# Performance work log

Measured on AMD Instinct MI355X. Metric: run time of the kernel, lower is better.

## Reference

```python
import jax, jax.numpy as jnp
import numpy as np

B, S, D, H = 4, 2048, 1024, 16
HD = D // H  # head_dim = 64


def setup_inputs() -> dict:
    key = jax.random.key(0)
    ks = jax.random.split(key, 9)
    sd = 1.0 / np.sqrt(D)
    x = jax.random.normal(ks[0], (B, S, D), dtype=jnp.float32)
    Wq = jax.random.normal(ks[1], (D, D), dtype=jnp.float32) * sd
    Wk = jax.random.normal(ks[2], (D, D), dtype=jnp.float32) * sd
    Wv = jax.random.normal(ks[3], (D, D), dtype=jnp.float32) * sd
    Wo = jax.random.normal(ks[4], (D, D), dtype=jnp.float32) * sd
    bq = jax.random.normal(ks[5], (D,), dtype=jnp.float32) * sd
    bk = jax.random.normal(ks[6], (D,), dtype=jnp.float32) * sd
    bv = jax.random.normal(ks[7], (D,), dtype=jnp.float32) * sd
    bo = jax.random.normal(ks[8], (D,), dtype=jnp.float32) * sd
    return {"x": x, "Wq": Wq, "bq": bq, "Wk": Wk, "bk": bk,
            "Wv": Wv, "bv": bv, "Wo": Wo, "bo": bo}


def reference(x, Wq, bq, Wk, bk, Wv, bv, Wo, bo):
    b, s, d = x.shape
    scale = jnp.float32(np.sqrt(HD))
    # projections, split into heads: (b, h, s, hd)
    def heads(y):
        return y.reshape(b, s, H, HD).transpose(0, 2, 1, 3)
    Q = heads(x @ Wq + bq)
    K = heads(x @ Wk + bk)
    V = heads(x @ Wv + bv)
    # (b, h, s, s) scores with causal mask
    scores = jnp.einsum('bhqd,bhkd->bhqk', Q, K) / scale
    causal = jnp.tril(jnp.ones((s, s), dtype=bool))
    scores = jnp.where(causal[None, None], scores, jnp.float32(-jnp.inf))
    probs = jax.nn.softmax(scores, axis=-1)
    out = jnp.einsum('bhqk,bhkd->bhqd', probs, V)
    out = out.transpose(0, 2, 1, 3).reshape(b, s, d)
    return out @ Wo + bo
```

## Files before the change

### kernel.cpp

```cpp
#include <hip/hip_runtime.h>
#include <hip/hip_bf16.h>
#include <cstdint>

typedef __bf16 bf16x8 __attribute__((ext_vector_type(8)));
typedef float f32x4 __attribute__((ext_vector_type(4)));
typedef float f32x16 __attribute__((ext_vector_type(16)));
typedef unsigned short u16t;

__device__ __forceinline__ u16t f2bf(float f) {
    uint32_t u = __builtin_bit_cast(uint32_t, f);
    u += 0x7FFF + ((u >> 16) & 1);
    return (u16t)(u >> 16);
}

constexpr int Bb = 4, Ss = 2048, Dd = 1024, Hh = 16;
constexpr int Mrows = Bb * Ss;
constexpr float NEG = -1e30f;

__global__ __launch_bounds__(256) void cvt_bf16(const float* __restrict__ in,
                                                u16t* __restrict__ out, int n) {
    int i = (blockIdx.x * 256 + threadIdx.x) * 4;
    if (i >= n) return;
    float4 v = *(const float4*)(in + i);
    u16t o[4] = {f2bf(v.x), f2bf(v.y), f2bf(v.z), f2bf(v.w)};
    *(ushort4*)(out + i) = *(ushort4*)o;
}

__global__ __launch_bounds__(256) void transpose_cvt4(const float* __restrict__ W0, u16t* __restrict__ T0,
                                                      const float* __restrict__ W1, u16t* __restrict__ T1,
                                                      const float* __restrict__ W2, u16t* __restrict__ T2,
                                                      const float* __restrict__ W3, u16t* __restrict__ T3) {
    __shared__ float tile[64][65];
    const float* W = blockIdx.z == 0 ? W0 : blockIdx.z == 1 ? W1 : blockIdx.z == 2 ? W2 : W3;
    u16t* WT       = blockIdx.z == 0 ? T0 : blockIdx.z == 1 ? T1 : blockIdx.z == 2 ? T2 : T3;
    int n0 = blockIdx.x * 64, k0 = blockIdx.y * 64;
    int c = threadIdx.x & 63, r0 = (threadIdx.x >> 6) * 16;
    for (int i = 0; i < 16; i++)
        tile[c][r0 + i] = W[(size_t)(k0 + r0 + i) * Dd + n0 + c];
    __syncthreads();
    for (int i = 0; i < 16; i++)
        WT[(size_t)(n0 + r0 + i) * Dd + k0 + c] = f2bf(tile[r0 + i][c]);
}

__global__ __launch_bounds__(256) void gemm_bt(const u16t* __restrict__ A,
                                               const u16t* __restrict__ BT,
                                               const float* __restrict__ bias,
                                               u16t* __restrict__ outBF,
                                               float* __restrict__ outF, int mode,
                                               float oscale) {
    __shared__ __align__(16) u16t Asm[128 * 32];
    __shared__ __align__(16) u16t Bsm[128 * 32];
    int tid = threadIdx.x, lane = tid & 63, w = tid >> 6;
    int wm = w >> 1, wn = w & 1;
    int ln = lane & 15, g = lane >> 4;
    int m0 = blockIdx.y * 128, n0 = blockIdx.x * 128;

    f32x4 acc[4][4] = {};

    int sr = w * 32 + (lane >> 2);
    int sc = (((lane & 3) ^ (sr & 3)) * 8);
    const u16t* Ag0 = A + (size_t)(m0 + sr) * Dd + sc;
    const u16t* Ag1 = A + (size_t)(m0 + sr + 16) * Dd + sc;
    const u16t* Bg0 = BT + (size_t)(n0 + sr) * Dd + sc;
    const u16t* Bg1 = BT + (size_t)(n0 + sr + 16) * Dd + sc;
    u16t* As0 = &Asm[(w * 32) * 32];
    u16t* As1 = &Asm[(w * 32 + 16) * 32];
    u16t* Bs0 = &Bsm[(w * 32) * 32];
    u16t* Bs1 = &Bsm[(w * 32 + 16) * 32];

    for (int k0 = 0; k0 < Dd; k0 += 32) {
        __syncthreads();
        __builtin_amdgcn_global_load_lds(Ag0 + k0, As0, 16, 0, 0);
        __builtin_amdgcn_global_load_lds(Ag1 + k0, As1, 16, 0, 0);
        __builtin_amdgcn_global_load_lds(Bg0 + k0, Bs0, 16, 0, 0);
        __builtin_amdgcn_global_load_lds(Bg1 + k0, Bs1, 16, 0, 0);
        __syncthreads();
        bf16x8 af[4], bf[4];
        #pragma unroll
        for (int i = 0; i < 4; i++) {
            int row = wm * 64 + i * 16 + ln;
            af[i] = *(const bf16x8*)&Asm[row * 32 + ((g ^ (row & 3)) * 8)];
        }
        #pragma unroll
        for (int j = 0; j < 4; j++) {
            int row = wn * 64 + j * 16 + ln;
            bf[j] = *(const bf16x8*)&Bsm[row * 32 + ((g ^ (row & 3)) * 8)];
        }
        #pragma unroll
        for (int i = 0; i < 4; i++)
            #pragma unroll
            for (int j = 0; j < 4; j++)
                acc[i][j] = __builtin_amdgcn_mfma_f32_16x16x32_bf16(af[i], bf[j], acc[i][j], 0, 0, 0);
    }

    #pragma unroll
    for (int i = 0; i < 4; i++) {
        #pragma unroll
        for (int j = 0; j < 4; j++) {
            int col = n0 + wn * 64 + j * 16 + ln;
            float bv = bias[col];
            int rowb = m0 + wm * 64 + i * 16 + g * 4;
            if (mode == 0) {
                for (int r = 0; r < 4; r++) {
                    int row = rowb + r;
                    float v = (acc[i][j][r] + bv) * oscale;
                    int b = row >> 11, s = row & 2047, h = col >> 6, hd = col & 63;
                    outBF[(((size_t)(b * Hh + h) << 11) + s) * 64 + hd] = f2bf(v);
                }
            } else if (mode == 1) {
                for (int r = 0; r < 4; r++)
                    outF[(size_t)(rowb + r) * Dd + col] = acc[i][j][r] + bv;
            } else {
                u16t pk4[4];
                for (int r = 0; r < 4; r++) pk4[r] = f2bf(acc[i][j][r] + bv);
                int b = rowb >> 11, s = rowb & 2047, h = col >> 6, hd = col & 63;
                *(ushort4*)(outBF + ((size_t)((b * Hh + h) * 64 + hd) << 11) + s) = *(ushort4*)pk4;
            }
        }
    }
}

__global__ __launch_bounds__(256) void attn(const u16t* __restrict__ Qh,
                                            const u16t* __restrict__ Kh,
                                            const u16t* __restrict__ Vt,
                                            u16t* __restrict__ Ob) {
    __shared__ __align__(16) u16t Ksm[2][64 * 64];
    __shared__ __align__(16) u16t Vsm[2][64 * 64];

    int tid = threadIdx.x, lane = tid & 63, w = tid >> 6;
    int l31 = lane & 31, hi = lane >> 5;
    int bh = blockIdx.y;
    int qx = blockIdx.x;
    if ((bh >> 4) & 1) qx = 15 - qx;
    int qb = qx * 128;
    int q0w = qb + w * 32;
    int qlane = q0w + l31;

    const u16t* Kb = Kh + (size_t)bh * Ss * 64;
    const u16t* Vb = Vt + (size_t)bh * 64 * Ss;

    bf16x8 qB[4];
    {
        const u16t* Qp = Qh + ((size_t)bh * Ss + qlane) * 64 + hi * 8;
        #pragma unroll
        for (int ks = 0; ks < 4; ks++)
            qB[ks] = *(const bf16x8*)(Qp + 16 * ks);
    }

    f32x16 oacc[2] = {};
    float m_run = NEG, l_run = 0.f;

    int nt = (qb >> 6) + 2;

    int sr0 = w * 16 + (lane >> 3);
    int sr1 = sr0 + 8;
    int sc0 = (((lane & 7) ^ (sr0 & 7) ^ ((sr0 >> 3) & 3)) * 8);
    int sc1 = (((lane & 7) ^ (sr1 & 7) ^ ((sr1 >> 3) & 3)) * 8);
    const u16t* Kg0 = Kb + (size_t)sr0 * 64 + sc0;
    const u16t* Kg1 = Kb + (size_t)sr1 * 64 + sc1;
    const u16t* Vg0 = Vb + (size_t)sr0 * Ss + sc0;
    const u16t* Vg1 = Vb + (size_t)sr1 * Ss + sc1;

    auto stage = [&](int buf, int t) {
        size_t koff = (size_t)t * 64 * 64;
        size_t voff = (size_t)t * 64;
        __builtin_amdgcn_global_load_lds(Kg0 + koff, &Ksm[buf][(w * 2 + 0) * 512], 16, 0, 0);
        __builtin_amdgcn_global_load_lds(Kg1 + koff, &Ksm[buf][(w * 2 + 1) * 512], 16, 0, 0);
        __builtin_amdgcn_global_load_lds(Vg0 + voff, &Vsm[buf][(w * 2 + 0) * 512], 16, 0, 0);
        __builtin_amdgcn_global_load_lds(Vg1 + voff, &Vsm[buf][(w * 2 + 1) * 512], 16, 0, 0);
    };

    stage(0, 0);
    __syncthreads();

    int swzr = (l31 & 7) ^ ((l31 >> 3) & 3);

    for (int t = 0; t < nt; t++) {
        int cur = t & 1;
        int kv0 = t << 6;
        if (t + 1 < nt) stage(cur ^ 1, t + 1);

        bool active = (kv0 <= q0w + 31);
        if (active) {
            f32x16 p0 = {}, p1 = {};
            __builtin_amdgcn_s_setprio(1);
            #pragma unroll
            for (int ks = 0; ks < 4; ks++) {
                int cc = (2 * ks + hi) ^ swzr;
                bf16x8 ka0 = *(const bf16x8*)&Ksm[cur][(size_t)l31 * 64 + cc * 8];
                bf16x8 ka1 = *(const bf16x8*)&Ksm[cur][(size_t)(32 + l31) * 64 + cc * 8];
                p0 = __builtin_amdgcn_mfma_f32_32x32x16_bf16(ka0, qB[ks], p0, 0, 0, 0);
                p1 = __builtin_amdgcn_mfma_f32_32x32x16_bf16(ka1, qB[ks], p1, 0, 0, 0);
            }
            __builtin_amdgcn_s_setprio(0);

            float pv[32];
            #pragma unroll
            for (int r = 0; r < 16; r++) { pv[r] = p0[r]; pv[16 + r] = p1[r]; }

            if (kv0 + 63 > q0w) {
                #pragma unroll
                for (int ti = 0; ti < 2; ti++)
                    #pragma unroll
                    for (int r = 0; r < 16; r++) {
                        int kvg = kv0 + 32 * ti + (r & 3) + 8 * (r >> 2) + 4 * hi;
                        if (kvg > qlane) pv[16 * ti + r] = NEG;
                    }
            }

            float mt = fmaxf(pv[0], pv[1]);
            #pragma unroll
            for (int r = 2; r < 32; r += 2)
                mt = fmaxf(fmaxf(mt, pv[r]), pv[r + 1]);
            mt = fmaxf(mt, __shfl_xor(mt, 32));
            if (__any(mt > m_run + 10.0f)) {
                float mn = fmaxf(m_run, mt);
                float al = __builtin_exp2f(m_run - mn);
                m_run = mn;
                l_run *= al;
                #pragma unroll
                for (int r = 0; r < 16; r++) { oacc[0][r] *= al; oacc[1][r] *= al; }
            }
            #pragma unroll
            for (int r = 0; r < 32; r++) pv[r] = __builtin_exp2f(pv[r] - m_run);
            float sa = 0.f, sb = 0.f, sc_ = 0.f, sd = 0.f;
            #pragma unroll
            for (int r = 0; r < 32; r += 4) {
                sa += pv[r]; sb += pv[r + 1]; sc_ += pv[r + 2]; sd += pv[r + 3];
            }
            float rsum = (sa + sb) + (sc_ + sd);
            rsum += __shfl_xor(rsum, 32);
            l_run += rsum;

            bf16x8 pb[4];
            #pragma unroll
            for (int half = 0; half < 2; half++) {
                const int base = 16 * half;
                uint32_t c0, c1, c2, c3;
                asm("v_cvt_pk_bf16_f32 %0, %1, %2" : "=v"(c0) : "v"(pv[base + 0]), "v"(pv[base + 1]));
                asm("v_cvt_pk_bf16_f32 %0, %1, %2" : "=v"(c1) : "v"(pv[base + 2]), "v"(pv[base + 3]));
                asm("v_cvt_pk_bf16_f32 %0, %1, %2" : "=v"(c2) : "v"(pv[base + 4]), "v"(pv[base + 5]));
                asm("v_cvt_pk_bf16_f32 %0, %1, %2" : "=v"(c3) : "v"(pv[base + 6]), "v"(pv[base + 7]));
                asm volatile("v_permlane32_swap_b32 %0, %1" : "+v"(c0), "+v"(c2));
                asm volatile("v_permlane32_swap_b32 %0, %1" : "+v"(c1), "+v"(c3));
                uint32_t w4[4] = {c0, c1, c2, c3};
                pb[2 * half] = *(bf16x8*)w4;
                uint32_t d0, d1, d2, d3;
                asm("v_cvt_pk_bf16_f32 %0, %1, %2" : "=v"(d0) : "v"(pv[base + 8]),  "v"(pv[base + 9]));
                asm("v_cvt_pk_bf16_f32 %0, %1, %2" : "=v"(d1) : "v"(pv[base + 10]), "v"(pv[base + 11]));
                asm("v_cvt_pk_bf16_f32 %0, %1, %2" : "=v"(d2) : "v"(pv[base + 12]), "v"(pv[base + 13]));
                asm("v_cvt_pk_bf16_f32 %0, %1, %2" : "=v"(d3) : "v"(pv[base + 14]), "v"(pv[base + 15]));
                asm volatile("v_permlane32_swap_b32 %0, %1" : "+v"(d0), "+v"(d2));
                asm volatile("v_permlane32_swap_b32 %0, %1" : "+v"(d1), "+v"(d3));
                uint32_t w5[4] = {d0, d1, d2, d3};
                pb[2 * half + 1] = *(bf16x8*)w5;
            }

            __builtin_amdgcn_s_setprio(1);
            #pragma unroll
            for (int dt = 0; dt < 2; dt++) {
                int drow = dt * 32 + l31;
                #pragma unroll
                for (int ks = 0; ks < 4; ks++) {
                    int cc = (2 * ks + hi) ^ swzr;
                    bf16x8 va = *(const bf16x8*)&Vsm[cur][(size_t)drow * 64 + cc * 8];
                    oacc[dt] = __builtin_amdgcn_mfma_f32_32x32x16_bf16(va, pb[ks], oacc[dt], 0, 0, 0);
                }
            }
            __builtin_amdgcn_s_setprio(0);
        }
        __syncthreads();
    }

    float inv = 1.0f / l_run;
    int b = bh >> 4, h = bh & 15;
    u16t* Op = Ob + ((size_t)(b * Ss + qlane)) * Dd + h * 64;
    #pragma unroll
    for (int dt = 0; dt < 2; dt++)
        #pragma unroll
        for (int rq = 0; rq < 4; rq++) {
            u16t pk4[4];
            #pragma unroll
            for (int j = 0; j < 4; j++) pk4[j] = f2bf(oacc[dt][rq * 4 + j] * inv);
            int d0 = dt * 32 + rq * 8 + hi * 4;
            *(ushort4*)(Op + d0) = *(ushort4*)pk4;
        }
}

extern "C" void kernel_launch(void* const* d_in, const int* in_sizes, int n_in,
                              void* d_out, int out_size, void* d_ws, size_t ws_size,
                              hipStream_t stream) {
    const float* x  = (const float*)d_in[0];
    const float* Wq = (const float*)d_in[1];
    const float* bq = (const float*)d_in[2];
    const float* Wk = (const float*)d_in[3];
    const float* bk = (const float*)d_in[4];
    const float* Wv = (const float*)d_in[5];
    const float* bv = (const float*)d_in[6];
    const float* Wo = (const float*)d_in[7];
    const float* bo = (const float*)d_in[8];

    char* ws = (char*)d_ws;
    size_t off = 0;
    auto alloc = [&](size_t bytes) { char* p = ws + off; off += (bytes + 255) & ~(size_t)255; return p; };
    u16t* xb  = (u16t*)alloc((size_t)Mrows * Dd * 2);
    u16t* WqT = (u16t*)alloc((size_t)Dd * Dd * 2);
    u16t* WkT = (u16t*)alloc((size_t)Dd * Dd * 2);
    u16t* WvT = (u16t*)alloc((size_t)Dd * Dd * 2);
    u16t* WoT = (u16t*)alloc((size_t)Dd * Dd * 2);
    u16t* Qh  = (u16t*)alloc((size_t)Mrows * Dd * 2);
    u16t* Kh  = (u16t*)alloc((size_t)Mrows * Dd * 2);
    u16t* Vtp = (u16t*)alloc((size_t)Mrows * Dd * 2);
    u16t* Ob  = (u16t*)alloc((size_t)Mrows * Dd * 2);

    int nx = Mrows * Dd;
    cvt_bf16<<<nx / (256 * 4), 256, 0, stream>>>(x, xb, nx);
    dim3 tg(16, 16, 4);
    transpose_cvt4<<<tg, 256, 0, stream>>>(Wq, WqT, Wk, WkT, Wv, WvT, Wo, WoT);

    constexpr float QSCALE = 0.125f * 1.44269504088896340736f;
    dim3 gg(Dd / 128, Mrows / 128);
    gemm_bt<<<gg, 256, 0, stream>>>(xb, WqT, bq, Qh, nullptr, 0, QSCALE);
    gemm_bt<<<gg, 256, 0, stream>>>(xb, WkT, bk, Kh, nullptr, 0, 1.0f);
    gemm_bt<<<gg, 256, 0, stream>>>(xb, WvT, bv, Vtp, nullptr, 2, 1.0f);

    dim3 ga(Ss / 128, Bb * Hh);
    attn<<<ga, 256, 0, stream>>>(Qh, Kh, Vtp, Ob);

    gemm_bt<<<gg, 256, 0, stream>>>(Ob, WoT, bo, nullptr, (float*)d_out, 1, 1.0f);
}
```

Baseline: 235.7 us.

## Fuse QKV projections into one GEMM, pair causal attention tiles per block, remap GEMM blocks

The three Q/K/V projection GEMMs become one launch over a concatenated 3072-wide transposed weight, with per-column-segment bias and output layout. The attention grid is halved and each block handles query tile i and its mirror 15-i in turn, so every block does the same amount of causal work. Both GEMMs also get a 1D grid with an XCD-aware block index remap meant to improve L2 locality. In exchange, the attention grid shrinks to 512 blocks, which may lower occupancy and overlap.

Measured after the change: 206.0 us. 1.14x faster.

```diff
diff --git a/kernel.cpp b/kernel.cpp
--- a/kernel.cpp
+++ b/kernel.cpp
@@ -16,6 +16,7 @@
 constexpr int Bb = 4, Ss = 2048, Dd = 1024, Hh = 16;
 constexpr int Mrows = Bb * Ss;
 constexpr float NEG = -1e30f;
+constexpr float QSCALE = 0.125f * 1.44269504088896340736f;
 
 __global__ __launch_bounds__(256) void cvt_bf16(const float* __restrict__ in,
                                                 u16t* __restrict__ out, int n) {
@@ -26,13 +27,16 @@
     *(ushort4*)(out + i) = *(ushort4*)o;
 }
 
-__global__ __launch_bounds__(256) void transpose_cvt4(const float* __restrict__ W0, u16t* __restrict__ T0,
-                                                      const float* __restrict__ W1, u16t* __restrict__ T1,
-                                                      const float* __restrict__ W2, u16t* __restrict__ T2,
-                                                      const float* __restrict__ W3, u16t* __restrict__ T3) {
+__global__ __launch_bounds__(256) void transpose_cvt4(const float* __restrict__ W0,
+                                                      const float* __restrict__ W1,
+                                                      const float* __restrict__ W2,
+                                                      const float* __restrict__ W3,
+                                                      u16t* __restrict__ Tqkv,
+                                                      u16t* __restrict__ To) {
     __shared__ float tile[64][65];
-    const float* W = blockIdx.z == 0 ? W0 : blockIdx.z == 1 ? W1 : blockIdx.z == 2 ? W2 : W3;
-    u16t* WT       = blockIdx.z == 0 ? T0 : blockIdx.z == 1 ? T1 : blockIdx.z == 2 ? T2 : T3;
+    int z = blockIdx.z;
+    const float* W = z == 0 ? W0 : z == 1 ? W1 : z == 2 ? W2 : W3;
+    u16t* WT = z < 3 ? Tqkv + (size_t)z * Dd * Dd : To;
     int n0 = blockIdx.x * 64, k0 = blockIdx.y * 64;
     int c = threadIdx.x & 63, r0 = (threadIdx.x >> 6) * 16;
     for (int i = 0; i < 16; i++)
@@ -42,18 +46,22 @@
         WT[(size_t)(n0 + r0 + i) * Dd + k0 + c] = f2bf(tile[r0 + i][c]);
 }
 
-__global__ __launch_bounds__(256) void gemm_bt(const u16t* __restrict__ A,
-                                               const u16t* __restrict__ BT,
-                                               const float* __restrict__ bias,
-                                               u16t* __restrict__ outBF,
-                                               float* __restrict__ outF, int mode,
-                                               float oscale) {
+__global__ __launch_bounds__(256) void gemm_qkv(const u16t* __restrict__ A,
+                                                const u16t* __restrict__ BT,
+                                                const float* __restrict__ bq,
+                                                const float* __restrict__ bk,
+                                                const float* __restrict__ bvv,
+                                                u16t* __restrict__ Qh,
+                                                u16t* __restrict__ Kh,
+                                                u16t* __restrict__ Vt) {
     __shared__ __align__(16) u16t Asm[128 * 32];
     __shared__ __align__(16) u16t Bsm[128 * 32];
     int tid = threadIdx.x, lane = tid & 63, w = tid >> 6;
     int wm = w >> 1, wn = w & 1;
     int ln = lane & 15, g = lane >> 4;
-    int m0 = blockIdx.y * 128, n0 = blockIdx.x * 128;
+    int bid = blockIdx.x;
+    int wg = (bid & 7) * 192 + (bid >> 3);
+    int n0 = (wg % 24) * 128, m0 = (wg / 24) * 128;
 
     f32x4 acc[4][4] = {};
 
@@ -98,24 +106,87 @@
         #pragma unroll
         for (int j = 0; j < 4; j++) {
             int col = n0 + wn * 64 + j * 16 + ln;
+            int seg = col >> 10, c1k = col & 1023;
+            float bias = seg == 0 ? bq[c1k] : seg == 1 ? bk[c1k] : bvv[c1k];
+            int rowb = m0 + wm * 64 + i * 16 + g * 4;
+            int b = rowb >> 11, s = rowb & 2047, h = c1k >> 6, hd = c1k & 63;
+            if (seg == 0) {
+                for (int r = 0; r < 4; r++) {
+                    float v = (acc[i][j][r] + bias) * QSCALE;
+                    Qh[((size_t)(b * Hh + h) * Ss + s + r) * 64 + hd] = f2bf(v);
+                }
+            } else if (seg == 1) {
+                for (int r = 0; r < 4; r++)
+                    Kh[((size_t)(b * Hh + h) * Ss + s + r) * 64 + hd] = f2bf(acc[i][j][r] + bias);
+            } else {
+                u16t pk4[4];
+                for (int r = 0; r < 4; r++) pk4[r] = f2bf(acc[i][j][r] + bias);
+                *(ushort4*)(Vt + ((size_t)((b * Hh + h) * 64 + hd) << 11) + s) = *(ushort4*)pk4;
+            }
+        }
+    }
+}
+
+__global__ __launch_bounds__(256) void gemm_o(const u16t* __restrict__ A,
+                                              const u16t* __restrict__ BT,
+                                              const float* __restrict__ bias,
+                                              float* __restrict__ outF) {
+    __shared__ __align__(16) u16t Asm[128 * 32];
+    __shared__ __align__(16) u16t Bsm[128 * 32];
+    int tid = threadIdx.x, lane = tid & 63, w = tid >> 6;
+    int wm = w >> 1, wn = w & 1;
+    int ln = lane & 15, g = lane >> 4;
+    int bid = blockIdx.x;
+    int wg = (bid & 7) * 64 + (bid >> 3);
+    int n0 = (wg & 7) * 128, m0 = (wg >> 3) * 128;
+
+    f32x4 acc[4][4] = {};
+
+    int sr = w * 32 + (lane >> 2);
+    int sc = (((lane & 3) ^ (sr & 3)) * 8);
+    const u16t* Ag0 = A + (size_t)(m0 + sr) * Dd + sc;
+    const u16t* Ag1 = A + (size_t)(m0 + sr + 16) * Dd + sc;
+    const u16t* Bg0 = BT + (size_t)(n0 + sr) * Dd + sc;
+    const u16t* Bg1 = BT + (size_t)(n0 + sr + 16) * Dd + sc;
+    u16t* As0 = &Asm[(w * 32) * 32];
+    u16t* As1 = &Asm[(w * 32 + 16) * 32];
+    u16t* Bs0 = &Bsm[(w * 32) * 32];
+    u16t* Bs1 = &Bsm[(w * 32 + 16) * 32];
+
+    for (int k0 = 0; k0 < Dd; k0 += 32) {
+        __syncthreads();
+        __builtin_amdgcn_global_load_lds(Ag0 + k0, As0, 16, 0, 0);
+        __builtin_amdgcn_global_load_lds(Ag1 + k0, As1, 16, 0, 0);
+        __builtin_amdgcn_global_load_lds(Bg0 + k0, Bs0, 16, 0, 0);
+        __builtin_amdgcn_global_load_lds(Bg1 + k0, Bs1, 16, 0, 0);
+        __syncthreads();
+        bf16x8 af[4], bf[4];
+        #pragma unroll
+        for (int i = 0; i < 4; i++) {
+            int row = wm * 64 + i * 16 + ln;
+            af[i] = *(const bf16x8*)&Asm[row * 32 + ((g ^ (row & 3)) * 8)];
+        }
+        #pragma unroll
+        for (int j = 0; j < 4; j++) {
+            int row = wn * 64 + j * 16 + ln;
+            bf[j] = *(const bf16x8*)&Bsm[row * 32 + ((g ^ (row & 3)) * 8)];
+        }
+        #pragma unroll
+        for (int i = 0; i < 4; i++)
+            #pragma unroll
+            for (int j = 0; j < 4; j++)
+                acc[i][j] = __builtin_amdgcn_mfma_f32_16x16x32_bf16(af[i], bf[j], acc[i][j], 0, 0, 0);
+    }
+
+    #pragma unroll
+    for (int i = 0; i < 4; i++) {
+        #pragma unroll
+        for (int j = 0; j < 4; j++) {
+            int col = n0 + wn * 64 + j * 16 + ln;
             float bv = bias[col];
             int rowb = m0 + wm * 64 + i * 16 + g * 4;
-            if (mode == 0) {
-                for (int r = 0; r < 4; r++) {
-                    int row = rowb + r;
-                    float v = (acc[i][j][r] + bv) * oscale;
-                    int b = row >> 11, s = row & 2047, h = col >> 6, hd = col & 63;
-                    outBF[(((size_t)(b * Hh + h) << 11) + s) * 64 + hd] = f2bf(v);
-                }
-            } else if (mode == 1) {
-                for (int r = 0; r < 4; r++)
-                    outF[(size_t)(rowb + r) * Dd + col] = acc[i][j][r] + bv;
-            } else {
-                u16t pk4[4];
-                for (int r = 0; r < 4; r++) pk4[r] = f2bf(acc[i][j][r] + bv);
-                int b = rowb >> 11, s = rowb & 2047, h = col >> 6, hd = col & 63;
-                *(ushort4*)(outBF + ((size_t)((b * Hh + h) * 64 + hd) << 11) + s) = *(ushort4*)pk4;
-            }
+            for (int r = 0; r < 4; r++)
+                outF[(size_t)(rowb + r) * Dd + col] = acc[i][j][r] + bv;
         }
     }
 }
@@ -130,27 +201,9 @@
     int tid = threadIdx.x, lane = tid & 63, w = tid >> 6;
     int l31 = lane & 31, hi = lane >> 5;
     int bh = blockIdx.y;
-    int qx = blockIdx.x;
-    if ((bh >> 4) & 1) qx = 15 - qx;
-    int qb = qx * 128;
-    int q0w = qb + w * 32;
-    int qlane = q0w + l31;
 
     const u16t* Kb = Kh + (size_t)bh * Ss * 64;
     const u16t* Vb = Vt + (size_t)bh * 64 * Ss;
-
-    bf16x8 qB[4];
-    {
-        const u16t* Qp = Qh + ((size_t)bh * Ss + qlane) * 64 + hi * 8;
-        #pragma unroll
-        for (int ks = 0; ks < 4; ks++)
-            qB[ks] = *(const bf16x8*)(Qp + 16 * ks);
-    }
-
-    f32x16 oacc[2] = {};
-    float m_run = NEG, l_run = 0.f;
-
-    int nt = (qb >> 6) + 2;
 
     int sr0 = w * 16 + (lane >> 3);
     int sr1 = sr0 + 8;
@@ -170,121 +223,140 @@
         __builtin_amdgcn_global_load_lds(Vg1 + voff, &Vsm[buf][(w * 2 + 1) * 512], 16, 0, 0);
     };
 
-    stage(0, 0);
-    __syncthreads();
-
     int swzr = (l31 & 7) ^ ((l31 >> 3) & 3);
 
-    for (int t = 0; t < nt; t++) {
-        int cur = t & 1;
-        int kv0 = t << 6;
-        if (t + 1 < nt) stage(cur ^ 1, t + 1);
-
-        bool active = (kv0 <= q0w + 31);
-        if (active) {
-            f32x16 p0 = {}, p1 = {};
-            __builtin_amdgcn_s_setprio(1);
+    for (int task = 0; task < 2; task++) {
+        int qx = task == 0 ? (int)blockIdx.x : 15 - (int)blockIdx.x;
+        int qb = qx * 128;
+        int q0w = qb + w * 32;
+        int qlane = q0w + l31;
+
+        bf16x8 qB[4];
+        {
+            const u16t* Qp = Qh + ((size_t)bh * Ss + qlane) * 64 + hi * 8;
             #pragma unroll
-            for (int ks = 0; ks < 4; ks++) {
-                int cc = (2 * ks + hi) ^ swzr;
-                bf16x8 ka0 = *(const bf16x8*)&Ksm[cur][(size_t)l31 * 64 + cc * 8];
-                bf16x8 ka1 = *(const bf16x8*)&Ksm[cur][(size_t)(32 + l31) * 64 + cc * 8];
-                p0 = __builtin_amdgcn_mfma_f32_32x32x16_bf16(ka0, qB[ks], p0, 0, 0, 0);
-                p1 = __builtin_amdgcn_mfma_f32_32x32x16_bf16(ka1, qB[ks], p1, 0, 0, 0);
-            }
-            __builtin_amdgcn_s_setprio(0);
-
-            float pv[32];
-            #pragma unroll
-            for (int r = 0; r < 16; r++) { pv[r] = p0[r]; pv[16 + r] = p1[r]; }
-
-            if (kv0 + 63 > q0w) {
-                #pragma unroll
-                for (int ti = 0; ti < 2; ti++)
-                    #pragma unroll
-                    for (int r = 0; r < 16; r++) {
-                        int kvg = kv0 + 32 * ti + (r & 3) + 8 * (r >> 2) + 4 * hi;
-                        if (kvg > qlane) pv[16 * ti + r] = NEG;
-                    }
-            }
-
-            float mt = fmaxf(pv[0], pv[1]);
-            #pragma unroll
-            for (int r = 2; r < 32; r += 2)
-                mt = fmaxf(fmaxf(mt, pv[r]), pv[r + 1]);
-            mt = fmaxf(mt, __shfl_xor(mt, 32));
-            if (__any(mt > m_run + 10.0f)) {
-                float mn = fmaxf(m_run, mt);
-                float al = __builtin_exp2f(m_run - mn);
-                m_run = mn;
-                l_run *= al;
-                #pragma unroll
-                for (int r = 0; r < 16; r++) { oacc[0][r] *= al; oacc[1][r] *= al; }
-            }
-            #pragma unroll
-            for (int r = 0; r < 32; r++) pv[r] = __builtin_exp2f(pv[r] - m_run);
-            float sa = 0.f, sb = 0.f, sc_ = 0.f, sd = 0.f;
-            #pragma unroll
-            for (int r = 0; r < 32; r += 4) {
-                sa += pv[r]; sb += pv[r + 1]; sc_ += pv[r + 2]; sd += pv[r + 3];
-            }
-            float rsum = (sa + sb) + (sc_ + sd);
-            rsum += __shfl_xor(rsum, 32);
-            l_run += rsum;
-
-            bf16x8 pb[4];
-            #pragma unroll
-            for (int half = 0; half < 2; half++) {
-                const int base = 16 * half;
-                uint32_t c0, c1, c2, c3;
-                asm("v_cvt_pk_bf16_f32 %0, %1, %2" : "=v"(c0) : "v"(pv[base + 0]), "v"(pv[base + 1]));
-                asm("v_cvt_pk_bf16_f32 %0, %1, %2" : "=v"(c1) : "v"(pv[base + 2]), "v"(pv[base + 3]));
-                asm("v_cvt_pk_bf16_f32 %0, %1, %2" : "=v"(c2) : "v"(pv[base + 4]), "v"(pv[base + 5]));
-                asm("v_cvt_pk_bf16_f32 %0, %1, %2" : "=v"(c3) : "v"(pv[base + 6]), "v"(pv[base + 7]));
-                asm volatile("v_permlane32_swap_b32 %0, %1" : "+v"(c0), "+v"(c2));
-                asm volatile("v_permlane32_swap_b32 %0, %1" : "+v"(c1), "+v"(c3));
-                uint32_t w4[4] = {c0, c1, c2, c3};
-                pb[2 * half] = *(bf16x8*)w4;
-                uint32_t d0, d1, d2, d3;
-                asm("v_cvt_pk_bf16_f32 %0, %1, %2" : "=v"(d0) : "v"(pv[base + 8]),  "v"(pv[base + 9]));
-                asm("v_cvt_pk_bf16_f32 %0, %1, %2" : "=v"(d1) : "v"(pv[base + 10]), "v"(pv[base + 11]));
-                asm("v_cvt_pk_bf16_f32 %0, %1, %2" : "=v"(d2) : "v"(pv[base + 12]), "v"(pv[base + 13]));
-                asm("v_cvt_pk_bf16_f32 %0, %1, %2" : "=v"(d3) : "v"(pv[base + 14]), "v"(pv[base + 15]));
-                asm volatile("v_permlane32_swap_b32 %0, %1" : "+v"(d0), "+v"(d2));
-                asm volatile("v_permlane32_swap_b32 %0, %1" : "+v"(d1), "+v"(d3));
-                uint32_t w5[4] = {d0, d1, d2, d3};
-                pb[2 * half + 1] = *(bf16x8*)w5;
-            }
-
-            __builtin_amdgcn_s_setprio(1);
-            #pragma unroll
-            for (int dt = 0; dt < 2; dt++) {
-                int drow = dt * 32 + l31;
+            for (int ks = 0; ks < 4; ks++)
+                qB[ks] = *(const bf16x8*)(Qp + 16 * ks);
+        }
+
+        f32x16 oacc[2] = {};
+        float m_run = NEG, l_run = 0.f;
+        int nt = (qb >> 6) + 2;
+
+        stage(0, 0);
+        __syncthreads();
+
+        for (int t = 0; t < nt; t++) {
+            int cur = t & 1;
+            int kv0 = t << 6;
+            if (t + 1 < nt) stage(cur ^ 1, t + 1);
+
+            bool active = (kv0 <= q0w + 31);
+            if (active) {
+                f32x16 p0 = {}, p1 = {};
+                __builtin_amdgcn_s_setprio(1);
                 #pragma unroll
                 for (int ks = 0; ks < 4; ks++) {
                     int cc = (2 * ks + hi) ^ swzr;
-                    bf16x8 va = *(const bf16x8*)&Vsm[cur][(size_t)drow * 64 + cc * 8];
-                    oacc[dt] = __builtin_amdgcn_mfma_f32_32x32x16_bf16(va, pb[ks], oacc[dt], 0, 0, 0);
-                }
+                    bf16x8 ka0 = *(const bf16x8*)&Ksm[cur][(size_t)l31 * 64 + cc * 8];
+                    bf16x8 ka1 = *(const bf16x8*)&Ksm[cur][(size_t)(32 + l31) * 64 + cc * 8];
+                    p0 = __builtin_amdgcn_mfma_f32_32x32x16_bf16(ka0, qB[ks], p0, 0, 0, 0);
+                    p1 = __builtin_amdgcn_mfma_f32_32x32x16_bf16(ka1, qB[ks], p1, 0, 0, 0);
+                }
+                __builtin_amdgcn_s_setprio(0);
+
+                float pv[32];
+                #pragma unroll
+                for (int r = 0; r < 16; r++) { pv[r] = p0[r]; pv[16 + r] = p1[r]; }
+
+                if (kv0 + 63 > q0w) {
+                    #pragma unroll
+                    for (int ti = 0; ti < 2; ti++)
+                        #pragma unroll
+                        for (int r = 0; r < 16; r++) {
+                            int kvg = kv0 + 32 * ti + (r & 3) + 8 * (r >> 2) + 4 * hi;
+                            if (kvg > qlane) pv[16 * ti + r] = NEG;
+                        }
+                }
+
+                float mt = fmaxf(pv[0], pv[1]);
+                #pragma unroll
+                for (int r = 2; r < 32; r += 2)
+                    mt = fmaxf(fmaxf(mt, pv[r]), pv[r + 1]);
+                mt = fmaxf(mt, __shfl_xor(mt, 32));
+                if (__any(mt > m_run + 10.0f)) {
+                    float mn = fmaxf(m_run, mt);
+                    float al = __builtin_exp2f(m_run - mn);
+                    m_run = mn;
+                    l_run *= al;
+                    #pragma unroll
+                    for (int r = 0; r < 16; r++) { oacc[0][r] *= al; oacc[1][r] *= al; }
+                }
+                #pragma unroll
+                for (int r = 0; r < 32; r++) pv[r] = __builtin_exp2f(pv[r] - m_run);
+                float sa = 0.f, sb = 0.f, sc_ = 0.f, sd = 0.f;
+                #pragma unroll
+                for (int r = 0; r < 32; r += 4) {
+                    sa += pv[r]; sb += pv[r + 1]; sc_ += pv[r + 2]; sd += pv[r + 3];
+                }
+                float rsum = (sa + sb) + (sc_ + sd);
+                rsum += __shfl_xor(rsum, 32);
+                l_run += rsum;
+
+                bf16x8 pb[4];
+                #pragma unroll
+                for (int half = 0; half < 2; half++) {
+                    const int base = 16 * half;
+                    uint32_t c0, c1, c2, c3;
+                    asm("v_cvt_pk_bf16_f32 %0, %1, %2" : "=v"(c0) : "v"(pv[base + 0]), "v"(pv[base + 1]));
+                    asm("v_cvt_pk_bf16_f32 %0, %1, %2" : "=v"(c1) : "v"(pv[base + 2]), "v"(pv[base + 3]));
+                    asm("v_cvt_pk_bf16_f32 %0, %1, %2" : "=v"(c2) : "v"(pv[base + 4]), "v"(pv[base + 5]));
+                    asm("v_cvt_pk_bf16_f32 %0, %1, %2" : "=v"(c3) : "v"(pv[base + 6]), "v"(pv[base + 7]));
+                    asm volatile("v_permlane32_swap_b32 %0, %1" : "+v"(c0), "+v"(c2));
+                    asm volatile("v_permlane32_swap_b32 %0, %1" : "+v"(c1), "+v"(c3));
+                    uint32_t w4[4] = {c0, c1, c2, c3};
+                    pb[2 * half] = *(bf16x8*)w4;
+                    uint32_t d0, d1, d2, d3;
+                    asm("v_cvt_pk_bf16_f32 %0, %1, %2" : "=v"(d0) : "v"(pv[base + 8]),  "v"(pv[base + 9]));
+                    asm("v_cvt_pk_bf16_f32 %0, %1, %2" : "=v"(d1) : "v"(pv[base + 10]), "v"(pv[base + 11]));
+                    asm("v_cvt_pk_bf16_f32 %0, %1, %2" : "=v"(d2) : "v"(pv[base + 12]), "v"(pv[base + 13]));
+                    asm("v_cvt_pk_bf16_f32 %0, %1, %2" : "=v"(d3) : "v"(pv[base + 14]), "v"(pv[base + 15]));
+                    asm volatile("v_permlane32_swap_b32 %0, %1" : "+v"(d0), "+v"(d2));
+                    asm volatile("v_permlane32_swap_b32 %0, %1" : "+v"(d1), "+v"(d3));
+                    uint32_t w5[4] = {d0, d1, d2, d3};
+                    pb[2 * half + 1] = *(bf16x8*)w5;
+                }
+
+                __builtin_amdgcn_s_setprio(1);
+                #pragma unroll
+                for (int dt = 0; dt < 2; dt++) {
+                    int drow = dt * 32 + l31;
+                    #pragma unroll
+                    for (int ks = 0; ks < 4; ks++) {
+                        int cc = (2 * ks + hi) ^ swzr;
+                        bf16x8 va = *(const bf16x8*)&Vsm[cur][(size_t)drow * 64 + cc * 8];
+                        oacc[dt] = __builtin_amdgcn_mfma_f32_32x32x16_bf16(va, pb[ks], oacc[dt], 0, 0, 0);
+                    }
+                }
+                __builtin_amdgcn_s_setprio(0);
             }
-            __builtin_amdgcn_s_setprio(0);
-        }
-        __syncthreads();
-    }
-
-    float inv = 1.0f / l_run;
-    int b = bh >> 4, h = bh & 15;
-    u16t* Op = Ob + ((size_t)(b * Ss + qlane)) * Dd + h * 64;
-    #pragma unroll
-    for (int dt = 0; dt < 2; dt++)
-        #pragma unroll
-        for (int rq = 0; rq < 4; rq++) {
-            u16t pk4[4];
+            __syncthreads();
+        }
+
+        float inv = 1.0f / l_run;
+        int b = bh >> 4, h = bh & 15;
+        u16t* Op = Ob + ((size_t)(b * Ss + qlane)) * Dd + h * 64;
+        #pragma unroll
+        for (int dt = 0; dt < 2; dt++)
             #pragma unroll
-            for (int j = 0; j < 4; j++) pk4[j] = f2bf(oacc[dt][rq * 4 + j] * inv);
-            int d0 = dt * 32 + rq * 8 + hi * 4;
-            *(ushort4*)(Op + d0) = *(ushort4*)pk4;
-        }
+            for (int rq = 0; rq < 4; rq++) {
+                u16t pk4[4];
+                #pragma unroll
+                for (int j = 0; j < 4; j++) pk4[j] = f2bf(oacc[dt][rq * 4 + j] * inv);
+                int d0 = dt * 32 + rq * 8 + hi * 4;
+                *(ushort4*)(Op + d0) = *(ushort4*)pk4;
+            }
+    }
 }
 
 extern "C" void kernel_launch(void* const* d_in, const int* in_sizes, int n_in,
@@ -303,29 +375,23 @@
     char* ws = (char*)d_ws;
     size_t off = 0;
     auto alloc = [&](size_t bytes) { char* p = ws + off; off += (bytes + 255) & ~(size_t)255; return p; };
-    u16t* xb  = (u16t*)alloc((size_t)Mrows * Dd * 2);
-    u16t* WqT = (u16t*)alloc((size_t)Dd * Dd * 2);
-    u16t* WkT = (u16t*)alloc((size_t)Dd * Dd * 2);
-    u16t* WvT = (u16t*)alloc((size_t)Dd * Dd * 2);
-    u16t* WoT = (u16t*)alloc((size_t)Dd * Dd * 2);
-    u16t* Qh  = (u16t*)alloc((size_t)Mrows * Dd * 2);
-    u16t* Kh  = (u16t*)alloc((size_t)Mrows * Dd * 2);
-    u16t* Vtp = (u16t*)alloc((size_t)Mrows * Dd * 2);
-    u16t* Ob  = (u16t*)alloc((size_t)Mrows * Dd * 2);
+    u16t* xb    = (u16t*)alloc((size_t)Mrows * Dd * 2);
+    u16t* WqkvT = (u16t*)alloc((size_t)3 * Dd * Dd * 2);
+    u16t* WoT   = (u16t*)alloc((size_t)Dd * Dd * 2);
+    u16t* Qh    = (u16t*)alloc((size_t)Mrows * Dd * 2);
+    u16t* Kh    = (u16t*)alloc((size_t)Mrows * Dd * 2);
+    u16t* Vtp   = (u16t*)alloc((size_t)Mrows * Dd * 2);
+    u16t* Ob    = (u16t*)alloc((size_t)Mrows * Dd * 2);
 
     int nx = Mrows * Dd;
     cvt_bf16<<<nx / (256 * 4), 256, 0, stream>>>(x, xb, nx);
     dim3 tg(16, 16, 4);
-    transpose_cvt4<<<tg, 256, 0, stream>>>(Wq, WqT, Wk, WkT, Wv, WvT, Wo, WoT);
-
-    constexpr float QSCALE = 0.125f * 1.44269504088896340736f;
-    dim3 gg(Dd / 128, Mrows / 128);
-    gemm_bt<<<gg, 256, 0, stream>>>(xb, WqT, bq, Qh, nullptr, 0, QSCALE);
-    gemm_bt<<<gg, 256, 0, stream>>>(xb, WkT, bk, Kh, nullptr, 0, 1.0f);
-    gemm_bt<<<gg, 256, 0, stream>>>(xb, WvT, bv, Vtp, nullptr, 2, 1.0f);
-
-    dim3 ga(Ss / 128, Bb * Hh);
+    transpose_cvt4<<<tg, 256, 0, stream>>>(Wq, Wk, Wv, Wo, WqkvT, WoT);
+
+    gemm_qkv<<<1536, 256, 0, stream>>>(xb, WqkvT, bq, bk, bv, Qh, Kh, Vtp);
+
+    dim3 ga(8, Bb * Hh);
     attn<<<ga, 256, 0, stream>>>(Qh, Kh, Vtp, Ob);
 
-    gemm_bt<<<gg, 256, 0, stream>>>(Ob, WoT, bo, nullptr, (float*)d_out, 1, 1.0f);
-}
+    gemm_o<<<512, 256, 0, stream>>>(Ob, WoT, bo, (float*)d_out);
+}
```
